# Optimization experiments

Hardware: AMD Instinct MI355X
Metric: run time of the kernel (lower is better)

Reference implementation:

```python
import jax, jax.numpy as jnp
import numpy as np

EMBED_DIM = 1024
NUM_HEADS = 16
HEAD_DIM = EMBED_DIM // NUM_HEADS
SCALE = HEAD_DIM ** -0.5
EPS = 1e-5


def _layer_norm(x, w, b):
    mu = jnp.mean(x, axis=-1, keepdims=True)
    var = jnp.mean(jnp.square(x - mu), axis=-1, keepdims=True)
    return (x - mu) * jax.lax.rsqrt(var + EPS) * w + b


def setup_inputs() -> dict:
    key = jax.random.key(0)
    ks = jax.random.split(key, 8)
    B, L, Lp, C = 8, 4096, 256, EMBED_DIM
    gain = 0.05  # xavier_uniform gain
    lim = gain * np.sqrt(6.0 / (C + C))
    return {
        "prompt": jax.random.normal(ks[0], (B, Lp, C), jnp.float32),
        "x": jax.random.normal(ks[1], (B, L, C), jnp.float32),
        "ln_q_w": jnp.ones((C,), jnp.float32),
        "ln_q_b": jnp.zeros((C,), jnp.float32),
        "ln_k_w": jnp.ones((C,), jnp.float32),
        "ln_k_b": jnp.zeros((C,), jnp.float32),
        "Wq": jax.random.uniform(ks[2], (C, C), jnp.float32, -lim, lim),
        "bq": jnp.zeros((C,), jnp.float32),
        "Wk": jax.random.uniform(ks[3], (C, C), jnp.float32, -lim, lim),
        "bk": jnp.zeros((C,), jnp.float32),
        "Wo": jax.random.uniform(ks[4], (C, C), jnp.float32, -lim, lim),
        "bo": jnp.zeros((C,), jnp.float32),
        "alpha": jnp.asarray(0.5, jnp.float32),
    }


def reference(prompt, x, ln_q_w, ln_q_b, ln_k_w, ln_k_b, Wq, bq, Wk, bk, Wo, bo, alpha):
    B, L, C = x.shape
    Lp = prompt.shape[1]
    H, D = NUM_HEADS, HEAD_DIM

    q = _layer_norm(prompt, ln_q_w, ln_q_b)
    k = _layer_norm(x, ln_k_w, ln_k_b)

    # torch Linear: y = x @ W^T + b (W is [out, in])
    Q = (q @ Wq.T + bq).reshape(B, Lp, H, D).transpose(0, 2, 1, 3)  # [B,H,Lp,D]
    K = (k @ Wk.T + bk).reshape(B, L, H, D).transpose(0, 2, 1, 3)   # [B,H,L,D]
    V = x.reshape(B, L, H, D).transpose(0, 2, 1, 3)                  # [B,H,L,D]

    Q = jnp.clip(Q, -10.0, 10.0)
    K = jnp.clip(K, -10.0, 10.0)

    scores = jnp.einsum('bhqd,bhkd->bhqk', Q, K) * SCALE
    scores = scores - jax.lax.stop_gradient(jnp.max(scores, axis=-1, keepdims=True))
    attn = jax.nn.softmax(scores, axis=-1)

    attn_out = jnp.einsum('bhqk,bhkd->bhqd', attn, V)
    attn_out = attn_out.transpose(0, 2, 1, 3).reshape(B, Lp, C)
    attn_out = attn_out @ Wo.T + bo

    global_signal = jnp.mean(attn_out, axis=1, keepdims=True)  # [B,1,C]
    a = jax.nn.sigmoid(alpha) * 0.3
    return x + a * global_signal
```

## Files before the change

### kernel.cpp

```cpp
#include <hip/hip_runtime.h>

typedef __attribute__((ext_vector_type(8))) short  short8;
typedef __attribute__((ext_vector_type(4))) float  floatx4;

#define NS 8

__device__ __forceinline__ unsigned short f2b(float f) {
  union { float f; unsigned u; } c; c.f = f;
  unsigned r = c.u + 0x7FFFu + ((c.u >> 16) & 1u);
  return (unsigned short)(r >> 16);
}

__device__ __forceinline__ float b2f(unsigned short u) {
  union { unsigned u; float f; } c; c.u = (unsigned)u << 16;
  return c.f;
}

__device__ __forceinline__ void async_copy16(const void* g, void* l) {
  __builtin_amdgcn_global_load_lds(
      (const __attribute__((address_space(1))) void*)g,
      (__attribute__((address_space(3))) void*)l, 16, 0, 0);
}

__global__ __launch_bounds__(256) void ln_bf16_kernel(
    const float* __restrict__ src, const float* __restrict__ w,
    const float* __restrict__ bias, unsigned short* __restrict__ dst) {
  const size_t row = blockIdx.x;
  const int t = threadIdx.x;
  const float4 v = *(const float4*)&src[row * 1024 + t * 4];
  float s = v.x + v.y + v.z + v.w;
  float q = v.x * v.x + v.y * v.y + v.z * v.z + v.w * v.w;
#pragma unroll
  for (int m = 32; m >= 1; m >>= 1) {
    s += __shfl_xor(s, m, 64);
    q += __shfl_xor(q, m, 64);
  }
  __shared__ float ss[4], sq[4];
  if ((t & 63) == 0) { ss[t >> 6] = s; sq[t >> 6] = q; }
  __syncthreads();
  s = ss[0] + ss[1] + ss[2] + ss[3];
  q = sq[0] + sq[1] + sq[2] + sq[3];
  const float mu = s * (1.f / 1024.f);
  const float var = q * (1.f / 1024.f) - mu * mu;
  const float rs = rsqrtf(var + 1e-5f);
  const float4 wv = *(const float4*)&w[t * 4];
  const float4 bv = *(const float4*)&bias[t * 4];
  ushort4 o;
  o.x = f2b((v.x - mu) * rs * wv.x + bv.x);
  o.y = f2b((v.y - mu) * rs * wv.y + bv.y);
  o.z = f2b((v.z - mu) * rs * wv.z + bv.z);
  o.w = f2b((v.w - mu) * rs * wv.w + bv.w);
  *(ushort4*)&dst[row * 1024 + t * 4] = o;
}

__global__ __launch_bounds__(256) void conv_bf16_kernel(
    const float* __restrict__ src, unsigned short* __restrict__ dst) {
  const size_t i = (size_t)blockIdx.x * 256 + threadIdx.x;
  const float4 v = ((const float4*)src)[i];
  ushort4 o;
  o.x = f2b(v.x); o.y = f2b(v.y); o.z = f2b(v.z); o.w = f2b(v.w);
  ((ushort4*)dst)[i] = o;
}

__global__ __launch_bounds__(256) void vtrans_kernel(
    const float* __restrict__ x, unsigned short* __restrict__ Vbf) {
  const int bh = blockIdx.x, kb = blockIdx.y;
  const int b = bh >> 4, h = bh & 15;
  const int t = threadIdx.x;
  const int d = t >> 2, kc = t & 3;
  const float* xp = x + (size_t)(b * 4096 + kb * 256) * 1024 + h * 64 + d;
  unsigned short* vp = Vbf + ((size_t)bh * 64 + d) * 4096 + kb * 256;
#pragma unroll
  for (int c = 0; c < 8; c++) {
    const int kk = c * 32 + kc * 8;
    short8 o;
#pragma unroll
    for (int j = 0; j < 8; j++)
      o[j] = (short)f2b(xp[(size_t)(kk + j) * 1024]);
    *(short8*)&vp[kk] = o;
  }
}

__global__ __launch_bounds__(256) void gemm_bt_kernel(
    const unsigned short* __restrict__ A, const unsigned short* __restrict__ W,
    const float* __restrict__ bias, unsigned short* __restrict__ out, int M) {
  __shared__ __align__(16) unsigned short As[128 * 64];
  __shared__ __align__(16) unsigned short Bs[128 * 64];
  const int tid = threadIdx.x;
  const int wave = tid >> 6, lane = tid & 63;
  const int quad = lane >> 4, l16 = lane & 15;
  const size_t m0 = (size_t)blockIdx.x * 128;
  const int n0 = blockIdx.y * 128;
  const int wm = (wave >> 1) * 64, wn = (wave & 1) * 64;
  const int r8 = lane >> 3, cvv = lane & 7;
  const int csrc = cvv ^ r8;

  floatx4 acc[4][4];
#pragma unroll
  for (int i = 0; i < 4; i++)
#pragma unroll
    for (int j = 0; j < 4; j++) acc[i][j] = (floatx4){0.f, 0.f, 0.f, 0.f};

  const unsigned short* gA = A + (m0 + wave * 32 + r8) * 1024 + csrc * 8;
  const unsigned short* gB = W + ((size_t)(n0 + wave * 32 + r8)) * 1024 + csrc * 8;

  for (int k0 = 0; k0 < 1024; k0 += 64) {
    __syncthreads();
#pragma unroll
    for (int it = 0; it < 4; ++it) {
      async_copy16(gA + (size_t)it * 8 * 1024 + k0, &As[(wave * 4 + it) * 512]);
      async_copy16(gB + (size_t)it * 8 * 1024 + k0, &Bs[(wave * 4 + it) * 512]);
    }
    __syncthreads();
#pragma unroll
    for (int kh = 0; kh < 2; ++kh) {
      short8 af[4], bf[4];
#pragma unroll
      for (int mi = 0; mi < 4; mi++) {
        int row = wm + mi * 16 + l16;
        af[mi] = *(const short8*)&As[row * 64 + (((kh * 4 + quad) ^ (row & 7)) * 8)];
      }
#pragma unroll
      for (int ni = 0; ni < 4; ni++) {
        int row = wn + ni * 16 + l16;
        bf[ni] = *(const short8*)&Bs[row * 64 + (((kh * 4 + quad) ^ (row & 7)) * 8)];
      }
#pragma unroll
      for (int mi = 0; mi < 4; mi++)
#pragma unroll
        for (int ni = 0; ni < 4; ni++)
          acc[mi][ni] = __builtin_amdgcn_mfma_f32_16x16x32_bf16(af[mi], bf[ni], acc[mi][ni], 0, 0, 0);
    }
  }
#pragma unroll
  for (int ni = 0; ni < 4; ni++) {
    int n = n0 + wn + ni * 16 + l16;
    float bv = bias[n];
#pragma unroll
    for (int mi = 0; mi < 4; mi++)
#pragma unroll
      for (int p = 0; p < 4; p++) {
        size_t m = m0 + wm + mi * 16 + quad * 4 + p;
        float v = acc[mi][ni][p] + bv;
        v = fminf(10.f, fmaxf(-10.f, v));
        out[m * 1024 + n] = f2b(v);
      }
  }
}

__global__ __launch_bounds__(256) void attn_kernel(
    const unsigned short* __restrict__ Qp,
    const unsigned short* __restrict__ Kp,
    const unsigned short* __restrict__ Vbf,
    unsigned short* __restrict__ Onum,
    float* __restrict__ lpart) {
  const int bh = blockIdx.x, split = blockIdx.y;
  const int b = bh >> 4, h = bh & 15;
  const int tid = threadIdx.x, wave = tid >> 6, lane = tid & 63;
  const int quad = lane >> 4, l16 = lane & 15;
  const int r8 = lane >> 3, cvv = lane & 7, csrc = cvv ^ r8;

  __shared__ __align__(16) unsigned short Ks[64 * 64];
  __shared__ __align__(16) unsigned short Vs[64 * 64];
  __shared__ __align__(16) unsigned short Pw[4][64 * 64];

  short8 qf[4][2];
#pragma unroll
  for (int mi = 0; mi < 4; mi++)
#pragma unroll
    for (int kh = 0; kh < 2; kh++)
      qf[mi][kh] = *(const short8*)&Qp[(size_t)(b * 256 + wave * 64 + mi * 16 + l16) * 1024 +
                                       h * 64 + kh * 32 + quad * 8];

  floatx4 oacc[4][4];
  floatx4 lacc[4];
#pragma unroll
  for (int i = 0; i < 4; i++) {
    lacc[i] = (floatx4){0.f, 0.f, 0.f, 0.f};
#pragma unroll
    for (int j = 0; j < 4; j++) oacc[i][j] = (floatx4){0.f, 0.f, 0.f, 0.f};
  }
  short8 ones;
#pragma unroll
  for (int j = 0; j < 8; j++) ones[j] = (short)0x3F80;

  const int kbase = split * (4096 / NS);
  const int rowbase = (wave & 1) * 32;
  const bool isK = (wave < 2);
  const unsigned short* gK = Kp + ((size_t)(b * 4096 + kbase + rowbase + r8)) * 1024 +
                             h * 64 + csrc * 8;
  const unsigned short* gV = Vbf + ((size_t)(bh * 64 + rowbase + r8)) * 4096 +
                             kbase + csrc * 8;

  for (int t = 0; t < (4096 / NS / 64); ++t) {
    __syncthreads();
    if (isK) {
#pragma unroll
      for (int it = 0; it < 4; ++it)
        async_copy16(gK + ((size_t)t * 64 + it * 8) * 1024, &Ks[(rowbase + it * 8) * 64]);
    } else {
#pragma unroll
      for (int it = 0; it < 4; ++it)
        async_copy16(gV + (size_t)it * 8 * 4096 + t * 64, &Vs[(rowbase + it * 8) * 64]);
    }
    __syncthreads();

    floatx4 sacc[4][4];
#pragma unroll
    for (int i = 0; i < 4; i++)
#pragma unroll
      for (int j = 0; j < 4; j++) sacc[i][j] = (floatx4){0.f, 0.f, 0.f, 0.f};
#pragma unroll
    for (int kh = 0; kh < 2; ++kh) {
      short8 kf[4];
#pragma unroll
      for (int ni = 0; ni < 4; ni++) {
        int row = ni * 16 + l16;
        kf[ni] = *(const short8*)&Ks[row * 64 + (((kh * 4 + quad) ^ (row & 7)) * 8)];
      }
#pragma unroll
      for (int mi = 0; mi < 4; mi++)
#pragma unroll
        for (int ni = 0; ni < 4; ni++)
          sacc[mi][ni] = __builtin_amdgcn_mfma_f32_16x16x32_bf16(qf[mi][kh], kf[ni], sacc[mi][ni], 0, 0, 0);
    }

#pragma unroll
    for (int mi = 0; mi < 4; mi++)
#pragma unroll
      for (int p = 0; p < 4; p++) {
        int q = mi * 16 + quad * 4 + p;
#pragma unroll
        for (int ni = 0; ni < 4; ni++) {
          float pv = __expf(sacc[mi][ni][p] * 0.125f);
          int kk = ni * 16 + l16;
          Pw[wave][q * 64 + (((kk >> 3) ^ (q & 7)) * 8) + (kk & 7)] = f2b(pv);
        }
      }

#pragma unroll
    for (int kh = 0; kh < 2; ++kh) {
      short8 pf[4], vf[4];
#pragma unroll
      for (int ni = 0; ni < 4; ni++) {
        int row = ni * 16 + l16;
        vf[ni] = *(const short8*)&Vs[row * 64 + (((kh * 4 + quad) ^ (row & 7)) * 8)];
      }
#pragma unroll
      for (int mi = 0; mi < 4; mi++) {
        int q = mi * 16 + l16;
        pf[mi] = *(const short8*)&Pw[wave][q * 64 + (((kh * 4 + quad) ^ (q & 7)) * 8)];
      }
#pragma unroll
      for (int mi = 0; mi < 4; mi++) {
#pragma unroll
        for (int ni = 0; ni < 4; ni++)
          oacc[mi][ni] = __builtin_amdgcn_mfma_f32_16x16x32_bf16(pf[mi], vf[ni], oacc[mi][ni], 0, 0, 0);
        lacc[mi] = __builtin_amdgcn_mfma_f32_16x16x32_bf16(pf[mi], ones, lacc[mi], 0, 0, 0);
      }
    }
  }

  unsigned short* Ob = Onum + ((size_t)bh * NS + split) * 256 * 64;
#pragma unroll
  for (int mi = 0; mi < 4; mi++)
#pragma unroll
    for (int ni = 0; ni < 4; ni++)
#pragma unroll
      for (int p = 0; p < 4; p++) {
        int q = wave * 64 + mi * 16 + quad * 4 + p;
        int d = ni * 16 + l16;
        Ob[q * 64 + d] = f2b(oacc[mi][ni][p]);
      }
  if (l16 == 0) {
    float* lb = lpart + ((size_t)bh * NS + split) * 256;
#pragma unroll
    for (int mi = 0; mi < 4; mi++)
#pragma unroll
      for (int p = 0; p < 4; p++)
        lb[wave * 64 + mi * 16 + quad * 4 + p] = lacc[mi][p];
  }
}

__global__ __launch_bounds__(256) void reduce_heads_kernel(
    const unsigned short* __restrict__ Onum, const float* __restrict__ lpart,
    float* __restrict__ ho) {
  const int bh = blockIdx.x;
  const int t = threadIdx.x;
  __shared__ float ls[256];
  __shared__ float red[4][64];
  float l = 0.f;
#pragma unroll
  for (int s = 0; s < NS; s++) l += lpart[((size_t)bh * NS + s) * 256 + t];
  ls[t] = l;
  __syncthreads();
  const int d = t & 63, qg = t >> 6;
  float part = 0.f;
  for (int qi = 0; qi < 64; ++qi) {
    int q = qg * 64 + qi;
    float on = 0.f;
#pragma unroll
    for (int s = 0; s < NS; s++)
      on += b2f(Onum[(((size_t)bh * NS + s) * 256 + q) * 64 + d]);
    part += on / ls[q];
  }
  red[qg][d] = part;
  __syncthreads();
  if (t < 64) {
    float v = (red[0][t] + red[1][t] + red[2][t] + red[3][t]) * (1.f / 256.f);
    int b = bh >> 4, h = bh & 15;
    ho[b * 1024 + h * 64 + t] = v;
  }
}

__global__ __launch_bounds__(256) void wo_proj_kernel(
    const float* __restrict__ ho, const float* __restrict__ Wo,
    const float* __restrict__ bo, float* __restrict__ gs) {
  const int b = blockIdx.x >> 2, cg = blockIdx.x & 3;
  const int t = threadIdx.x;
  __shared__ float hs[1024];
#pragma unroll
  for (int i = 0; i < 4; i++) hs[t + i * 256] = ho[b * 1024 + t + i * 256];
  __syncthreads();
  const int c = cg * 256 + t;
  const float* wrow = Wo + (size_t)c * 1024;
  float acc = bo[c];
  for (int k = 0; k < 1024; k += 4) {
    float4 w4 = *(const float4*)&wrow[k];
    acc += w4.x * hs[k] + w4.y * hs[k + 1] + w4.z * hs[k + 2] + w4.w * hs[k + 3];
  }
  gs[b * 1024 + c] = acc;
}

__global__ __launch_bounds__(256) void final_add_kernel(
    const float* __restrict__ x, const float* __restrict__ gs,
    const float* __restrict__ alpha, float* __restrict__ out) {
  const float a = 0.3f / (1.f + __expf(-alpha[0]));
  const size_t i4 = (size_t)blockIdx.x * 256 + threadIdx.x;
  const float4 xv = ((const float4*)x)[i4];
  const float4 g = *(const float4*)&gs[(i4 >> 20) * 1024 + (i4 & 255) * 4];
  float4 o;
  o.x = xv.x + a * g.x; o.y = xv.y + a * g.y;
  o.z = xv.z + a * g.z; o.w = xv.w + a * g.w;
  ((float4*)out)[i4] = o;
}

extern "C" void kernel_launch(void* const* d_in, const int* in_sizes, int n_in,
                              void* d_out, int out_size, void* d_ws, size_t ws_size,
                              hipStream_t stream) {
  const float* prompt = (const float*)d_in[0];
  const float* x      = (const float*)d_in[1];
  const float* lnqw   = (const float*)d_in[2];
  const float* lnqb   = (const float*)d_in[3];
  const float* lnkw   = (const float*)d_in[4];
  const float* lnkb   = (const float*)d_in[5];
  const float* Wq     = (const float*)d_in[6];
  const float* bq     = (const float*)d_in[7];
  const float* Wk     = (const float*)d_in[8];
  const float* bk     = (const float*)d_in[9];
  const float* Wo     = (const float*)d_in[10];
  const float* bo     = (const float*)d_in[11];
  const float* alpha  = (const float*)d_in[12];
  float* out = (float*)d_out;

  char* ws = (char*)d_ws;
  unsigned short* kln = (unsigned short*)(ws + 0);
  unsigned short* Vbf = (unsigned short*)(ws + 0);
  unsigned short* qln = (unsigned short*)(ws + 67108864);
  unsigned short* Wqb = (unsigned short*)(ws + 71303168);
  unsigned short* Wkb = (unsigned short*)(ws + 73400320);
  unsigned short* Qp  = (unsigned short*)(ws + 75497472);
  float* lpart        = (float*)(ws + 79691776);
  float* ho           = (float*)(ws + 80740352);
  float* gs           = (float*)(ws + 80773120);

  char* ob = (char*)d_out;
  unsigned short* Kp   = (unsigned short*)(ob + 0);
  unsigned short* Onum = (unsigned short*)(ob + 67108864);

  ln_bf16_kernel<<<32768, 256, 0, stream>>>(x, lnkw, lnkb, kln);
  ln_bf16_kernel<<<2048, 256, 0, stream>>>(prompt, lnqw, lnqb, qln);
  conv_bf16_kernel<<<1024, 256, 0, stream>>>(Wq, Wqb);
  conv_bf16_kernel<<<1024, 256, 0, stream>>>(Wk, Wkb);
  gemm_bt_kernel<<<dim3(16, 8), 256, 0, stream>>>(qln, Wqb, bq, Qp, 2048);
  gemm_bt_kernel<<<dim3(256, 8), 256, 0, stream>>>(kln, Wkb, bk, Kp, 32768);
  vtrans_kernel<<<dim3(128, 16), 256, 0, stream>>>(x, Vbf);
  attn_kernel<<<dim3(128, NS), 256, 0, stream>>>(Qp, Kp, Vbf, Onum, lpart);
  reduce_heads_kernel<<<128, 256, 0, stream>>>(Onum, lpart, ho);
  wo_proj_kernel<<<32, 256, 0, stream>>>(ho, Wo, bo, gs);
  final_add_kernel<<<32768, 256, 0, stream>>>(x, gs, alpha, out);
}
```

Before: 596.1 us.

## Register-prefetch K/V tiles, fuse score/exp with packed bf16 P writes, vectorize head reduce

Replaces the async global-to-LDS copies with register staging, so the next K/V tile is loaded into registers while the current tile is computed, then stored to LDS at the top of the next iteration. The QK^T loop is restructured per key column block with swapped MFMA operands, which lets each lane hold consecutive keys and write exp values as packed bf16 pairs via v_cvt_pk_bf16_f32 with exp2f, instead of scalar f2b stores. The head reduction kernel is vectorized to ushort4 loads with a 16-way partial reduction. This adds register pressure and relies on the transposed MFMA output layout matching the Pw swizzle.

```diff
diff --git a/kernel.cpp b/kernel.cpp
--- a/kernel.cpp
+++ b/kernel.cpp
@@ -2,6 +2,7 @@
 
 typedef __attribute__((ext_vector_type(8))) short  short8;
 typedef __attribute__((ext_vector_type(4))) float  floatx4;
+typedef __attribute__((ext_vector_type(2))) unsigned int uint2v;
 
 #define NS 8
 
@@ -14,6 +15,12 @@
 __device__ __forceinline__ float b2f(unsigned short u) {
   union { unsigned u; float f; } c; c.u = (unsigned)u << 16;
   return c.f;
+}
+
+__device__ __forceinline__ unsigned cvt_pk_bf16(float a, float b) {
+  unsigned r;
+  asm("v_cvt_pk_bf16_f32 %0, %1, %2" : "=v"(r) : "v"(a), "v"(b));
+  return r;
 }
 
 __device__ __forceinline__ void async_copy16(const void* g, void* l) {
@@ -192,51 +199,70 @@
   const unsigned short* gV = Vbf + ((size_t)(bh * 64 + rowbase + r8)) * 4096 +
                              kbase + csrc * 8;
 
-  for (int t = 0; t < (4096 / NS / 64); ++t) {
+  const int T = 4096 / NS / 64;
+
+  uint4 stg[4];
+  if (isK) {
+#pragma unroll
+    for (int it = 0; it < 4; ++it)
+      stg[it] = *(const uint4*)&gK[((size_t)it * 8) * 1024];
+  } else {
+#pragma unroll
+    for (int it = 0; it < 4; ++it)
+      stg[it] = *(const uint4*)&gV[(size_t)it * 8 * 4096];
+  }
+
+  for (int t = 0; t < T; ++t) {
     __syncthreads();
     if (isK) {
 #pragma unroll
       for (int it = 0; it < 4; ++it)
-        async_copy16(gK + ((size_t)t * 64 + it * 8) * 1024, &Ks[(rowbase + it * 8) * 64]);
+        *(uint4*)((char*)Ks + (rowbase + it * 8) * 128 + lane * 16) = stg[it];
     } else {
 #pragma unroll
       for (int it = 0; it < 4; ++it)
-        async_copy16(gV + (size_t)it * 8 * 4096 + t * 64, &Vs[(rowbase + it * 8) * 64]);
+        *(uint4*)((char*)Vs + (rowbase + it * 8) * 128 + lane * 16) = stg[it];
     }
     __syncthreads();
-
-    floatx4 sacc[4][4];
-#pragma unroll
-    for (int i = 0; i < 4; i++)
-#pragma unroll
-      for (int j = 0; j < 4; j++) sacc[i][j] = (floatx4){0.f, 0.f, 0.f, 0.f};
-#pragma unroll
-    for (int kh = 0; kh < 2; ++kh) {
-      short8 kf[4];
-#pragma unroll
-      for (int ni = 0; ni < 4; ni++) {
-        int row = ni * 16 + l16;
-        kf[ni] = *(const short8*)&Ks[row * 64 + (((kh * 4 + quad) ^ (row & 7)) * 8)];
-      }
-#pragma unroll
-      for (int mi = 0; mi < 4; mi++)
-#pragma unroll
-        for (int ni = 0; ni < 4; ni++)
-          sacc[mi][ni] = __builtin_amdgcn_mfma_f32_16x16x32_bf16(qf[mi][kh], kf[ni], sacc[mi][ni], 0, 0, 0);
-    }
-
-#pragma unroll
-    for (int mi = 0; mi < 4; mi++)
-#pragma unroll
-      for (int p = 0; p < 4; p++) {
-        int q = mi * 16 + quad * 4 + p;
-#pragma unroll
-        for (int ni = 0; ni < 4; ni++) {
-          float pv = __expf(sacc[mi][ni][p] * 0.125f);
-          int kk = ni * 16 + l16;
-          Pw[wave][q * 64 + (((kk >> 3) ^ (q & 7)) * 8) + (kk & 7)] = f2b(pv);
-        }
-      }
+    if (t + 1 < T) {
+      if (isK) {
+#pragma unroll
+        for (int it = 0; it < 4; ++it)
+          stg[it] = *(const uint4*)&gK[((size_t)(t + 1) * 64 + it * 8) * 1024];
+      } else {
+#pragma unroll
+        for (int it = 0; it < 4; ++it)
+          stg[it] = *(const uint4*)&gV[(size_t)it * 8 * 4096 + (t + 1) * 64];
+      }
+    }
+
+#pragma unroll
+    for (int ni = 0; ni < 4; ++ni) {
+      const int krow = ni * 16 + l16;
+      const short8 kf0 = *(const short8*)&Ks[krow * 64 + (((0 + quad) ^ (krow & 7)) * 8)];
+      const short8 kf1 = *(const short8*)&Ks[krow * 64 + (((4 + quad) ^ (krow & 7)) * 8)];
+      floatx4 st[4];
+#pragma unroll
+      for (int mi = 0; mi < 4; ++mi) {
+        st[mi] = (floatx4){0.f, 0.f, 0.f, 0.f};
+        st[mi] = __builtin_amdgcn_mfma_f32_16x16x32_bf16(kf0, qf[mi][0], st[mi], 0, 0, 0);
+        st[mi] = __builtin_amdgcn_mfma_f32_16x16x32_bf16(kf1, qf[mi][1], st[mi], 0, 0, 0);
+      }
+#pragma unroll
+      for (int mi = 0; mi < 4; ++mi) {
+        const float C = 0.18033688011112042f;
+        float e0 = exp2f(st[mi][0] * C);
+        float e1 = exp2f(st[mi][1] * C);
+        float e2 = exp2f(st[mi][2] * C);
+        float e3 = exp2f(st[mi][3] * C);
+        unsigned lo = cvt_pk_bf16(e0, e1);
+        unsigned hi = cvt_pk_bf16(e2, e3);
+        const int q = mi * 16 + l16;
+        const int chunk = (ni * 2 + (quad >> 1)) ^ (q & 7);
+        uint2v w; w.x = lo; w.y = hi;
+        *(uint2v*)&Pw[wave][q * 64 + chunk * 8 + (quad & 1) * 4] = w;
+      }
+    }
 
 #pragma unroll
     for (int kh = 0; kh < 2; ++kh) {
@@ -288,26 +314,33 @@
   const int bh = blockIdx.x;
   const int t = threadIdx.x;
   __shared__ float ls[256];
-  __shared__ float red[4][64];
+  __shared__ float red[16][64];
   float l = 0.f;
 #pragma unroll
   for (int s = 0; s < NS; s++) l += lpart[((size_t)bh * NS + s) * 256 + t];
   ls[t] = l;
   __syncthreads();
-  const int d = t & 63, qg = t >> 6;
-  float part = 0.f;
-  for (int qi = 0; qi < 64; ++qi) {
-    int q = qg * 64 + qi;
-    float on = 0.f;
-#pragma unroll
-    for (int s = 0; s < NS; s++)
-      on += b2f(Onum[(((size_t)bh * NS + s) * 256 + q) * 64 + d]);
-    part += on / ls[q];
-  }
-  red[qg][d] = part;
+  const int d4 = t & 15, qg = t >> 4;
+  float4 part = {0.f, 0.f, 0.f, 0.f};
+  for (int qi = 0; qi < 16; ++qi) {
+    int q = qg * 16 + qi;
+    float4 on = {0.f, 0.f, 0.f, 0.f};
+#pragma unroll
+    for (int s = 0; s < NS; s++) {
+      ushort4 v = *(const ushort4*)&Onum[(((size_t)bh * NS + s) * 256 + q) * 64 + d4 * 4];
+      on.x += b2f(v.x); on.y += b2f(v.y); on.z += b2f(v.z); on.w += b2f(v.w);
+    }
+    const float rl = 1.f / ls[q];
+    part.x += on.x * rl; part.y += on.y * rl;
+    part.z += on.z * rl; part.w += on.w * rl;
+  }
+  *(float4*)&red[qg][d4 * 4] = part;
   __syncthreads();
   if (t < 64) {
-    float v = (red[0][t] + red[1][t] + red[2][t] + red[3][t]) * (1.f / 256.f);
+    float v = 0.f;
+#pragma unroll
+    for (int r = 0; r < 16; ++r) v += red[r][t];
+    v *= (1.f / 256.f);
     int b = bh >> 4, h = bh & 15;
     ho[b * 1024 + h * 64 + t] = v;
   }
```

New measurement: 565.8 us. 1.05x faster.
